# Performance work log

Hardware: AMD Instinct MI355X
Metric: run time of the kernel (lower is better)

The kernel has to match this reference:

```python
import math
import jax, jax.numpy as jnp
import numpy as np

B, C, HI, WI = 64, 3, 224, 224
H, W, UR, UT = 32, 64, 10, 10
R_MIN, R_MAX = 0.01, 0.6


def setup_inputs() -> dict:
    key = jax.random.key(0)
    kx, kl = jax.random.split(key)
    # log-spaced radii and uniform angles -> polar sample grid [Hg, Wg, 2] (x, y)
    sample_r = np.exp(np.linspace(math.log(R_MIN), math.log(R_MAX), UR * H)).astype(np.float32)
    angles = (2.0 * np.pi * np.arange(W * UT) / (W * UT)).astype(np.float32)
    grid_2d = np.stack(
        [sample_r[:, None] * np.cos(angles)[None, :],
         sample_r[:, None] * np.sin(angles)[None, :]], axis=-1
    ).astype(np.float32)
    x = jax.random.normal(kx, (B, C, HI, WI), dtype=jnp.float32)
    l_t_prev = jax.random.uniform(kl, (B, 2), minval=-0.3, maxval=0.3, dtype=jnp.float32)
    return {"x": x, "l_t_prev": l_t_prev, "grid_2d": jnp.asarray(grid_2d)}


def _grid_sample_bilinear_zeros(x, grid):
    # x: [B,C,Hi,Wi]; grid: [B,Hg,Wg,2] normalized (x,y) in [-1,1]
    # matches torch.grid_sample(mode='bilinear', padding_mode='zeros', align_corners=False)
    _, _, Hi, Wi = x.shape
    gx, gy = grid[..., 0], grid[..., 1]
    ix = ((gx + 1.0) * Wi - 1.0) * 0.5
    iy = ((gy + 1.0) * Hi - 1.0) * 0.5
    x0 = jnp.floor(ix)
    y0 = jnp.floor(iy)
    fx = ix - x0
    fy = iy - y0
    x0i = x0.astype(jnp.int32)
    y0i = y0.astype(jnp.int32)

    def gather(img, yy, xx):  # img [C,Hi,Wi]; yy,xx [Hg,Wg]
        return img[:, yy, xx]  # [C,Hg,Wg]

    out = jnp.zeros((x.shape[0], x.shape[1]) + grid.shape[1:3], dtype=x.dtype)
    for dy in (0, 1):
        for dx in (0, 1):
            xi = x0i + dx
            yi = y0i + dy
            wgt = (fx if dx else (1.0 - fx)) * (fy if dy else (1.0 - fy))
            valid = (xi >= 0) & (xi < Wi) & (yi >= 0) & (yi < Hi)
            xc = jnp.clip(xi, 0, Wi - 1)
            yc = jnp.clip(yi, 0, Hi - 1)
            v = jax.vmap(gather)(x, yc, xc)  # [B,C,Hg,Wg]
            out = out + v * (wgt * valid.astype(x.dtype))[:, None, :, :]
    return out


def reference(x, l_t_prev, grid_2d):
    # shift polar grid by glimpse center
    grid = l_t_prev[:, None, None, :] + grid_2d[None]  # [B,Hg,Wg,2]
    sampled = _grid_sample_bilinear_zeros(x, grid)      # [B,C,Hg,Wg]
    b, c, hg, wg = sampled.shape
    # AvgPool2d with kernel [UR, UT], stride [UR, UT]
    pooled = sampled.reshape(b, c, hg // UR, UR, wg // UT, UT).mean(axis=(3, 5))
    return pooled  # [B,C,H,W]
```

## Files before the change

kernel.cpp:

```cpp
#include <hip/hip_runtime.h>

#define Bx 64
#define Cx 3
#define HIx 224
#define WIx 224
#define HWx (HIx*WIx)
#define Hx 32
#define Wx 64
#define LDS_PX 3456

__device__ __forceinline__ unsigned f2bf(float f) {
    unsigned u = __float_as_uint(f);
    return ((u + 0x7fffu + ((u >> 16) & 1u)) >> 16);
}
__device__ __forceinline__ float bf_lo(unsigned u) { return __uint_as_float(u << 16); }
__device__ __forceinline__ float bf_hi(unsigned u) { return __uint_as_float(u & 0xffff0000u); }

__global__ __launch_bounds__(256)
void sample_analytic(const float* __restrict__ xg,
                     const float* __restrict__ lt,
                     float* __restrict__ out) {
    __shared__ uint2 tile[LDS_PX];

    int bx = blockIdx.x;
    int xcd  = bx & 7;
    int sub8 = (bx >> 3) & 7;
    int b    = xcd * 8 + sub8;
    int rest = bx >> 6;
    int sec  = rest >> 1;
    int h    = rest & 1;

    float lx = lt[2 * b];
    float ly = lt[2 * b + 1];
    float cxc = fmaf(lx, 112.f, 111.5f);
    float cyc = fmaf(ly, 112.f, 111.5f);

    const float DTH = 0.00981747704f;
    float t0a = (float)(40 * sec)      * DTH;
    float t1a = (float)(40 * sec + 39) * DTH;
    float c0s = __cosf(t0a), s0s = __sinf(t0a);
    float c1s = __cosf(t1a), s1s = __sinf(t1a);
    float rA = h ? 8.70f  : 1.12f;
    float rB = h ? 67.2f  : 8.66f;
    float xa = rA * c0s, xb_ = rA * c1s, xc = rB * c0s, xd = rB * c1s;
    float ya = rA * s0s, yb_ = rA * s1s, yc = rB * s0s, yd = rB * s1s;
    float xmn = fminf(fminf(xa, xb_), fminf(xc, xd));
    float xmx = fmaxf(fmaxf(xa, xb_), fmaxf(xc, xd));
    float ymn = fminf(fminf(ya, yb_), fminf(yc, yd));
    float ymx = fmaxf(fmaxf(ya, yb_), fmaxf(yc, yd));
    int xlo = (int)floorf(cxc + xmn) - 1;
    int xhi = (int)floorf(cxc + xmx) + 2;
    int ylo = (int)floorf(cyc + ymn) - 1;
    int yhi = (int)floorf(cyc + ymx) + 2;
    int Wb = (xhi - xlo + 1) | 1;

    int wid  = threadIdx.x >> 6;
    int lane = threadIdx.x & 63;
    const float* xb0 = xg + (size_t)b * Cx * HWx;
    for (int y = ylo + wid; y <= yhi; y += 4) {
        const float* row = xb0 + y * WIx;
        int lbase = (y - ylo) * Wb - xlo;
        for (int x = xlo + lane; x <= xhi; x += 64) {
            float v0 = row[x];
            float v1 = row[x + HWx];
            float v2 = row[x + 2 * HWx];
            uint2 p;
            p.x = f2bf(v0) | (f2bf(v1) << 16);
            p.y = f2bf(v2);
            tile[lbase + x] = p;
        }
    }
    __syncthreads();

    int ap = threadIdx.x & 1;
    int rp = (threadIdx.x >> 1) & 1;
    int pxi = threadIdx.x >> 2;
    int oh = h * 16 + (pxi >> 2);
    int ow = sec * 4 + (pxi & 3);

    const float DL = 0.0128349359f;
    const float L0 = -4.60517019f;
    float R0p = 112.f * __expf(fmaf((float)(oh * 10), DL, L0));
    const float KG[10] = {1.f,          1.01291766f, 1.02600217f, 1.03925572f, 1.05268048f,
                          1.06627866f,  1.08005247f, 1.09400417f, 1.10813601f, 1.12245030f};
    float rr[5];
#pragma unroll
    for (int k = 0; k < 5; ++k) rr[k] = R0p * (rp ? KG[2 * k + 1] : KG[2 * k]);

    float th0 = (float)(ow * 10) * DTH;
    float cth = __cosf(th0), sth = __sinf(th0);
    const float C[10] = {1.f,         0.99995181f, 0.99980724f, 0.99956631f, 0.99922903f,
                         0.99879546f, 0.99826561f, 0.99763955f, 0.99691733f, 0.99609904f};
    const float S[10] = {0.f,         0.00981732f, 0.01963369f, 0.02944817f, 0.03925982f,
                         0.04906767f, 0.05887080f, 0.06866826f, 0.07845910f, 0.08824237f};
    float u[5], v[5];
#pragma unroll
    for (int jp = 0; jp < 5; ++jp) {
        int jj = 2 * jp + ap;
        u[jp] = fmaf(cth, C[jj], -sth * S[jj]);
        v[jp] = fmaf(sth, C[jj],  cth * S[jj]);
    }

    float cxl = cxc - (float)xlo;
    float cyl = cyc - (float)ylo;

    float a0 = 0.f, a1 = 0.f, a2 = 0.f;
#pragma unroll
    for (int k = 0; k < 5; ++k) {
        float rg = rr[k];
#pragma unroll
        for (int jp = 0; jp < 5; ++jp) {
            float ix = fmaf(rg, u[jp], cxl);
            float iy = fmaf(rg, v[jp], cyl);
            int x0 = (int)ix, y0 = (int)iy;
            float fx = ix - (float)x0;
            float fy = iy - (float)y0;
            const uint2* p = &tile[y0 * Wb + x0];
            uint2 q00 = p[0], q01 = p[1];
            uint2 q10 = p[Wb], q11 = p[Wb + 1];
            float m00 = fmaf(fx, bf_lo(q01.x) - bf_lo(q00.x), bf_lo(q00.x));
            float m01 = fmaf(fx, bf_hi(q01.x) - bf_hi(q00.x), bf_hi(q00.x));
            float m02 = fmaf(fx, bf_lo(q01.y) - bf_lo(q00.y), bf_lo(q00.y));
            float m10 = fmaf(fx, bf_lo(q11.x) - bf_lo(q10.x), bf_lo(q10.x));
            float m11 = fmaf(fx, bf_hi(q11.x) - bf_hi(q10.x), bf_hi(q10.x));
            float m12 = fmaf(fx, bf_lo(q11.y) - bf_lo(q10.y), bf_lo(q10.y));
            a0 += fmaf(fy, m10 - m00, m00);
            a1 += fmaf(fy, m11 - m01, m01);
            a2 += fmaf(fy, m12 - m02, m02);
        }
    }

    a0 += __shfl_xor(a0, 1); a0 += __shfl_xor(a0, 2);
    a1 += __shfl_xor(a1, 1); a1 += __shfl_xor(a1, 2);
    a2 += __shfl_xor(a2, 1); a2 += __shfl_xor(a2, 2);

    if ((threadIdx.x & 3) == 0) {
        const float sc = 0.01f;
        int obase = b * (Cx * Hx * Wx) + oh * Wx + ow;
        out[obase]               = a0 * sc;
        out[obase + Hx * Wx]     = a1 * sc;
        out[obase + 2 * Hx * Wx] = a2 * sc;
    }
}

extern "C" void kernel_launch(void* const* d_in, const int* in_sizes, int n_in,
                              void* d_out, int out_size, void* d_ws, size_t ws_size,
                              hipStream_t stream) {
    const float* x  = (const float*)d_in[0];
    const float* lt = (const float*)d_in[1];
    float* out = (float*)d_out;
    (void)d_ws; (void)ws_size;

    sample_analytic<<<2048, 256, 0, stream>>>(x, lt, out);
}
```

Baseline: 96.03 us.

## Retile outer polar region into 8x8 sectors to shrink per-block LDS footprint

Splits the work per block differently. The inner radial half keeps 16x4 output sectors, while the outer half is split into two radial bands of 8 rows by 8 angular columns. This shrinks the bounding box of image pixels each block stages into LDS, so the LDS array is cut and more blocks may fit per CU. The grid size is unchanged. Bounding-box radii are hand-tuned constants, so any sample falling outside the staged tile would read wrong LDS data.

```diff
diff --git a/kernel.cpp b/kernel.cpp
--- a/kernel.cpp
+++ b/kernel.cpp
@@ -7,7 +7,7 @@
 #define HWx (HIx*WIx)
 #define Hx 32
 #define Wx 64
-#define LDS_PX 3456
+#define LDS_PX 2944
 
 __device__ __forceinline__ unsigned f2bf(float f) {
     unsigned u = __float_as_uint(f);
@@ -23,25 +23,35 @@
     __shared__ uint2 tile[LDS_PX];
 
     int bx = blockIdx.x;
-    int xcd  = bx & 7;
-    int sub8 = (bx >> 3) & 7;
-    int b    = xcd * 8 + sub8;
-    int rest = bx >> 6;
-    int sec  = rest >> 1;
-    int h    = rest & 1;
+    int b  = ((bx & 7) << 3) + ((bx >> 3) & 7);
+    int rt = bx >> 6;
+
+    const float DTH = 0.00981747704f;
+    float rA, rB, t0a, t1a;
+    int oh0, owbase, pair;
+    if (rt < 16) {
+        int sec = rt;
+        t0a = (float)(40 * sec)      * DTH;
+        t1a = (float)(40 * sec + 39) * DTH;
+        rA = 1.12f;  rB = 8.66f;
+        oh0 = 0; owbase = sec * 4; pair = 0;
+    } else {
+        int rr = rt - 16;
+        int p = rr >> 1, q = rr & 1;
+        t0a = (float)(80 * p)      * DTH;
+        t1a = (float)(80 * p + 79) * DTH;
+        rA = q ? 24.30f : 8.70f;
+        rB = q ? 67.25f : 24.10f;
+        oh0 = 16 + q * 8; owbase = p * 8; pair = 1;
+    }
 
     float lx = lt[2 * b];
     float ly = lt[2 * b + 1];
     float cxc = fmaf(lx, 112.f, 111.5f);
     float cyc = fmaf(ly, 112.f, 111.5f);
 
-    const float DTH = 0.00981747704f;
-    float t0a = (float)(40 * sec)      * DTH;
-    float t1a = (float)(40 * sec + 39) * DTH;
     float c0s = __cosf(t0a), s0s = __sinf(t0a);
     float c1s = __cosf(t1a), s1s = __sinf(t1a);
-    float rA = h ? 8.70f  : 1.12f;
-    float rB = h ? 67.2f  : 8.66f;
     float xa = rA * c0s, xb_ = rA * c1s, xc = rB * c0s, xd = rB * c1s;
     float ya = rA * s0s, yb_ = rA * s1s, yc = rB * s0s, yd = rB * s1s;
     float xmn = fminf(fminf(xa, xb_), fminf(xc, xd));
@@ -75,17 +85,18 @@
     int ap = threadIdx.x & 1;
     int rp = (threadIdx.x >> 1) & 1;
     int pxi = threadIdx.x >> 2;
-    int oh = h * 16 + (pxi >> 2);
-    int ow = sec * 4 + (pxi & 3);
+    int oh, ow;
+    if (pair) { oh = oh0 + (pxi >> 3); ow = owbase + (pxi & 7); }
+    else      { oh = oh0 + (pxi >> 2); ow = owbase + (pxi & 3); }
 
     const float DL = 0.0128349359f;
     const float L0 = -4.60517019f;
     float R0p = 112.f * __expf(fmaf((float)(oh * 10), DL, L0));
     const float KG[10] = {1.f,          1.01291766f, 1.02600217f, 1.03925572f, 1.05268048f,
                           1.06627866f,  1.08005247f, 1.09400417f, 1.10813601f, 1.12245030f};
-    float rr[5];
+    float rr5[5];
 #pragma unroll
-    for (int k = 0; k < 5; ++k) rr[k] = R0p * (rp ? KG[2 * k + 1] : KG[2 * k]);
+    for (int k = 0; k < 5; ++k) rr5[k] = R0p * (rp ? KG[2 * k + 1] : KG[2 * k]);
 
     float th0 = (float)(ow * 10) * DTH;
     float cth = __cosf(th0), sth = __sinf(th0);
@@ -107,7 +118,7 @@
     float a0 = 0.f, a1 = 0.f, a2 = 0.f;
 #pragma unroll
     for (int k = 0; k < 5; ++k) {
-        float rg = rr[k];
+        float rg = rr5[k];
 #pragma unroll
         for (int jp = 0; jp < 5; ++jp) {
             float ix = fmaf(rg, u[jp], cxl);
```

New measurement: 95.21 us. Within noise of the previous version (-0.9%).
